# Performance work log

Measured on AMD Instinct MI355X. Metric: run time of the kernel, lower is better.

Reference implementation:

```python
import jax, jax.numpy as jnp
import numpy as np

B, M, KD, VD = 512, 2048, 64, 64
MAX_IT = M - 1  # iteration[0].max().item() in the torch module; made static here


def setup_inputs() -> dict:
    key = jax.random.key(0)
    ks = jax.random.split(key, 8)
    new_key = jax.random.normal(ks[0], (B, KD), dtype=jnp.float32)
    new_value = jax.random.normal(ks[1], (B, VD), dtype=jnp.float32)
    key_memory = jax.random.normal(ks[2], (B, M, KD), dtype=jnp.float32)
    value_memory = jax.random.normal(ks[3], (B, M, VD), dtype=jnp.float32)
    gate = jax.random.normal(ks[4], (B, KD + 1), dtype=jnp.float32)
    iteration = jax.random.randint(ks[5], (B, 1), 1, MAX_IT + 1).astype(jnp.int64 if jax.config.jax_enable_x64 else jnp.int32)
    iteration = iteration.at[0, 0].set(MAX_IT)  # guarantee max == MAX_IT (faithful to .max().item())
    conf_w = jax.random.normal(ks[6], (1, 1), dtype=jnp.float32) * 0.1  # FCNM 1->1 linear weight
    conf_b = jnp.zeros((1,), dtype=jnp.float32)                          # FCNM 1->1 linear bias
    return {
        "new_key": new_key, "new_value": new_value,
        "key_memory": key_memory, "value_memory": value_memory,
        "gate": gate, "conf_w": conf_w, "conf_b": conf_b,
        "iteration": iteration, "max_it": MAX_IT,
    }


def reference(new_key, new_value, key_memory, value_memory, gate, conf_w, conf_b, iteration, max_it):
    b, m, kd = key_memory.shape
    vd = value_memory.shape[-1]
    it = iteration[:, 0]  # [B]

    # --- masked similarity read (vectorized form of the masked_select/scatter_ path) ---
    # memory_mask[b, n] = (n <= iteration[b])
    memory_mask = (jnp.arange(m)[None, :] <= it[:, None]).astype(key_memory.dtype)[..., None]  # [B,M,1]
    not_first = it > 1  # rows where the read actually happens; others stay zero

    vm = value_memory * memory_mask                              # [B,M,VD]
    sim = jnp.einsum('bnd,bd->bn', vm, new_value)                # [B,M]
    wv = jax.nn.softmax(sim, axis=-1)[..., None]                 # [B,M,1]
    conf = jax.nn.sigmoid(sim[..., None] * conf_w[0, 0] + conf_b[0])  # [B,M,1] (1->1 linear + sigmoid)
    km_plus_conf = jnp.concatenate([key_memory, conf], axis=-1)  # [B,M,KD+1]
    read = jnp.sum(wv * km_plus_conf, axis=1)                    # [B,KD+1]
    read = jax.nn.sigmoid(gate) * read
    new_read_key_plus_conf = jnp.where(not_first[:, None], read, jnp.zeros((), dtype=read.dtype))

    # --- resize memory to max_it + 1 slots and scatter-write the new key/value ---
    zeros_k = jnp.zeros((b, 1, kd), dtype=key_memory.dtype)
    zeros_v = jnp.zeros((b, 1, vd), dtype=value_memory.dtype)
    new_key_memory = jnp.concatenate([key_memory[:, :max_it], zeros_k], axis=1)    # [B,max_it+1,KD]
    new_value_memory = jnp.concatenate([value_memory[:, :max_it], zeros_v], axis=1)
    bidx = jnp.arange(b)
    new_key_memory = new_key_memory.at[bidx, it].set(new_key)
    new_value_memory = new_value_memory.at[bidx, it].set(new_value)

    return new_key_memory, new_value_memory, new_read_key_plus_conf
```

## Files before the change

### kernel.cpp

```cpp
#include <hip/hip_runtime.h>
#include <math.h>

#define KD 64
#define VD 64
#define RPB 256
#define RPL 16

typedef float vfloat4 __attribute__((ext_vector_type(4)));

__device__ __forceinline__ vfloat4 ntload4(const float* p) {
    return __builtin_nontemporal_load(reinterpret_cast<const vfloat4*>(p));
}
__device__ __forceinline__ void ntstore4(float* p, vfloat4 v) {
    __builtin_nontemporal_store(v, reinterpret_cast<vfloat4*>(p));
}

__global__ __launch_bounds__(256) void fused_stream(
    const float* __restrict__ value_memory,
    const float* __restrict__ key_memory,
    const float* __restrict__ new_value,
    const float* __restrict__ new_key,
    const int*   __restrict__ iteration,
    const float* __restrict__ conf_w,
    const float* __restrict__ conf_b,
    float* __restrict__ new_value_memory,
    float* __restrict__ new_key_memory,
    float* __restrict__ Spart,
    float* __restrict__ PCpart,
    float* __restrict__ pread,
    int M, int max_it)
{
    const int blocks_per_batch = M / RPB;
    const int b     = blockIdx.x / blocks_per_batch;
    const int split = blockIdx.x % blocks_per_batch;
    const int row0  = split * RPB;
    const int it    = iteration[b];
    const float cw  = conf_w[0], cb = conf_b[0];

    const int tid = threadIdx.x;
    const int l   = tid & 63;
    const int w   = tid >> 6;
    const int c4  = (l & 15) * 4;
    const int rsub = w * 4 + (l >> 4);

    const vfloat4 nv = *reinterpret_cast<const vfloat4*>(new_value + (size_t)b * VD + c4);
    const vfloat4 nk = *reinterpret_cast<const vfloat4*>(new_key   + (size_t)b * KD + c4);
    const float* vmb  = value_memory     + (size_t)b * M * VD;
    const float* kmb  = key_memory       + (size_t)b * M * KD;
    float*       ovmb = new_value_memory + (size_t)b * M * VD;
    float*       okmb = new_key_memory   + (size_t)b * M * KD;

    float sloc = 0.f, pcloc = 0.f;
    vfloat4 acc = (vfloat4){0.f, 0.f, 0.f, 0.f};

    #pragma unroll
    for (int i = 0; i < RPL; ++i) {
        const int n = row0 + rsub + i * 16;
        const size_t off = (size_t)n * 64 + c4;

        vfloat4 v = ntload4(vmb + off);
        vfloat4 k = ntload4(kmb + off);

        float part = fmaf(v.x, nv.x, fmaf(v.y, nv.y, fmaf(v.z, nv.z, v.w * nv.w)));
        part += __shfl_xor(part, 1);
        part += __shfl_xor(part, 2);
        part += __shfl_xor(part, 4);
        part += __shfl_xor(part, 8);

        const float s = (n <= it) ? part : 0.0f;
        const float p = expf(s);
        sloc  += p;
        pcloc += p * (1.0f / (1.0f + expf(-(s * cw + cb))));

        acc.x = fmaf(p, k.x, acc.x); acc.y = fmaf(p, k.y, acc.y);
        acc.z = fmaf(p, k.z, acc.z); acc.w = fmaf(p, k.w, acc.w);

        vfloat4 ovv, ovk;
        if (n == it)          { ovv = nv; ovk = nk; }
        else if (n == max_it) { ovv = (vfloat4){0,0,0,0}; ovk = (vfloat4){0,0,0,0}; }
        else                  { ovv = v;  ovk = k; }
        ntstore4(ovmb + off, ovv);
        ntstore4(okmb + off, ovk);
    }

    sloc  += __shfl_xor(sloc, 16);  sloc  += __shfl_xor(sloc, 32);
    pcloc += __shfl_xor(pcloc, 16); pcloc += __shfl_xor(pcloc, 32);

    acc.x += __shfl_xor(acc.x, 16); acc.y += __shfl_xor(acc.y, 16);
    acc.z += __shfl_xor(acc.z, 16); acc.w += __shfl_xor(acc.w, 16);
    acc.x += __shfl_xor(acc.x, 32); acc.y += __shfl_xor(acc.y, 32);
    acc.z += __shfl_xor(acc.z, 32); acc.w += __shfl_xor(acc.w, 32);

    __shared__ float sS[4], sPC[4];
    __shared__ float racc[4][64];
    if (l == 0) { sS[w] = sloc; sPC[w] = pcloc; }
    if (l < 16) {
        racc[w][c4 + 0] = acc.x; racc[w][c4 + 1] = acc.y;
        racc[w][c4 + 2] = acc.z; racc[w][c4 + 3] = acc.w;
    }
    __syncthreads();
    if (tid == 0) {
        Spart [b * blocks_per_batch + split] = sS[0] + sS[1] + sS[2] + sS[3];
        PCpart[b * blocks_per_batch + split] = sPC[0] + sPC[1] + sPC[2] + sPC[3];
    }
    if (tid < 64) {
        const float sumk = racc[0][tid] + racc[1][tid] + racc[2][tid] + racc[3][tid];
        pread[((size_t)b * blocks_per_batch + split) * 64 + tid] = sumk;
    }
}

__global__ __launch_bounds__(256) void k3_finalize(
    const float* __restrict__ pread,
    const float* __restrict__ Spart,
    const float* __restrict__ PCpart,
    const float* __restrict__ gate,
    const int*   __restrict__ iteration,
    float* __restrict__ out_read,
    int B, int splits)
{
    const int idx = blockIdx.x * 256 + threadIdx.x;
    if (idx >= B * (KD + 1)) return;
    const int b = idx / (KD + 1);
    const int k = idx % (KD + 1);

    float S = 0.f;
    for (int s = 0; s < splits; ++s) S += Spart[b * splits + s];

    float r = 0.f;
    if (k < KD) {
        for (int s = 0; s < splits; ++s)
            r += pread[((size_t)b * splits + s) * 64 + k];
    } else {
        for (int s = 0; s < splits; ++s) r += PCpart[b * splits + s];
    }
    const float g = gate[(size_t)b * (KD + 1) + k];
    float val = (1.0f / (1.0f + expf(-g))) * (r / S);
    if (iteration[b] <= 1) val = 0.0f;
    out_read[idx] = val;
}

extern "C" void kernel_launch(void* const* d_in, const int* in_sizes, int n_in,
                              void* d_out, int out_size, void* d_ws, size_t ws_size,
                              hipStream_t stream) {
    const float* new_key      = (const float*)d_in[0];
    const float* new_value    = (const float*)d_in[1];
    const float* key_memory   = (const float*)d_in[2];
    const float* value_memory = (const float*)d_in[3];
    const float* gate         = (const float*)d_in[4];
    const float* conf_w       = (const float*)d_in[5];
    const float* conf_b       = (const float*)d_in[6];
    const int*   iteration    = (const int*)d_in[7];

    const int B = in_sizes[0] / KD;
    const int M = in_sizes[2] / in_sizes[0];
    const int max_it = M - 1;
    const int splits = M / RPB;

    float* out_km   = (float*)d_out;
    float* out_vm   = out_km + (size_t)B * M * KD;
    float* out_read = out_vm + (size_t)B * M * VD;

    float* Spart  = (float*)d_ws;
    float* PCpart = Spart + (size_t)B * splits;
    float* pread  = PCpart + (size_t)B * splits;

    fused_stream<<<B * splits, 256, 0, stream>>>(
        value_memory, key_memory, new_value, new_key, iteration,
        conf_w, conf_b, out_vm, out_km, Spart, PCpart, pread, M, max_it);

    const int total = B * (KD + 1);
    k3_finalize<<<(total + 255) / 256, 256, 0, stream>>>(
        pread, Spart, PCpart, gate, iteration, out_read, B, splits);
}
```

Before: 204.4 us.

## Fuse read finalize into one block-per-batch streaming kernel with split value/key passes

Replaces the two-kernel split-reduction design with a single kernel that uses one 1024-thread block per batch row, so the softmax normalisation and gate can be applied in-block and the workspace round-trip plus second launch go away. The value memory is streamed first and exp weights are stashed in shared memory, then key memory is streamed in a second loop that reuses them. Scatter writes of new rows and the zero row are peeled out of the loops, and exp/sigmoid switch to fast intrinsics. Only 512 large blocks are launched, with 8KB+ of LDS each, which may limit occupancy and latency hiding relative to the earlier 4096-block grid.

```diff
diff --git a/kernel.cpp b/kernel.cpp
--- a/kernel.cpp
+++ b/kernel.cpp
@@ -3,8 +3,8 @@
 
 #define KD 64
 #define VD 64
-#define RPB 256
-#define RPL 16
+#define MM 2048
+#define NITER (MM / 64)
 
 typedef float vfloat4 __attribute__((ext_vector_type(4)));
 
@@ -14,8 +14,11 @@
 __device__ __forceinline__ void ntstore4(float* p, vfloat4 v) {
     __builtin_nontemporal_store(v, reinterpret_cast<vfloat4*>(p));
 }
+__device__ __forceinline__ float fastsig(float x) {
+    return __builtin_amdgcn_rcpf(1.0f + __expf(-x));
+}
 
-__global__ __launch_bounds__(256) void fused_stream(
+__global__ __launch_bounds__(1024) void fused_all(
     const float* __restrict__ value_memory,
     const float* __restrict__ key_memory,
     const float* __restrict__ new_value,
@@ -23,43 +26,42 @@
     const int*   __restrict__ iteration,
     const float* __restrict__ conf_w,
     const float* __restrict__ conf_b,
+    const float* __restrict__ gate,
     float* __restrict__ new_value_memory,
     float* __restrict__ new_key_memory,
-    float* __restrict__ Spart,
-    float* __restrict__ PCpart,
-    float* __restrict__ pread,
-    int M, int max_it)
+    float* __restrict__ out_read,
+    int max_it)
 {
-    const int blocks_per_batch = M / RPB;
-    const int b     = blockIdx.x / blocks_per_batch;
-    const int split = blockIdx.x % blocks_per_batch;
-    const int row0  = split * RPB;
-    const int it    = iteration[b];
-    const float cw  = conf_w[0], cb = conf_b[0];
-
+    const int b   = blockIdx.x;
     const int tid = threadIdx.x;
     const int l   = tid & 63;
     const int w   = tid >> 6;
     const int c4  = (l & 15) * 4;
-    const int rsub = w * 4 + (l >> 4);
+    const int g   = w * 4 + (l >> 4);
+
+    const int it   = iteration[b];
+    const float cw = conf_w[0], cb = conf_b[0];
+
+    __shared__ float pS[MM];
+    __shared__ float sS[16], sPC[16];
+    __shared__ float racc[16][64];
 
     const vfloat4 nv = *reinterpret_cast<const vfloat4*>(new_value + (size_t)b * VD + c4);
     const vfloat4 nk = *reinterpret_cast<const vfloat4*>(new_key   + (size_t)b * KD + c4);
-    const float* vmb  = value_memory     + (size_t)b * M * VD;
-    const float* kmb  = key_memory       + (size_t)b * M * KD;
-    float*       ovmb = new_value_memory + (size_t)b * M * VD;
-    float*       okmb = new_key_memory   + (size_t)b * M * KD;
+    const vfloat4 z4 = (vfloat4){0.f, 0.f, 0.f, 0.f};
+
+    const size_t base = (size_t)g * 64 + c4;
+    const float* vmb  = value_memory     + (size_t)b * MM * VD;
+    const float* kmb  = key_memory       + (size_t)b * MM * KD;
+    float*       ovmb = new_value_memory + (size_t)b * MM * VD;
+    float*       okmb = new_key_memory   + (size_t)b * MM * KD;
 
     float sloc = 0.f, pcloc = 0.f;
-    vfloat4 acc = (vfloat4){0.f, 0.f, 0.f, 0.f};
-
-    #pragma unroll
-    for (int i = 0; i < RPL; ++i) {
-        const int n = row0 + rsub + i * 16;
-        const size_t off = (size_t)n * 64 + c4;
-
+    #pragma unroll 8
+    for (int i = 0; i < NITER; ++i) {
+        const int n = i * 64 + g;
+        const size_t off = base + (size_t)i * 64 * 64;
         vfloat4 v = ntload4(vmb + off);
-        vfloat4 k = ntload4(kmb + off);
 
         float part = fmaf(v.x, nv.x, fmaf(v.y, nv.y, fmaf(v.z, nv.z, v.w * nv.w)));
         part += __shfl_xor(part, 1);
@@ -68,75 +70,61 @@
         part += __shfl_xor(part, 8);
 
         const float s = (n <= it) ? part : 0.0f;
-        const float p = expf(s);
+        const float p = __expf(s);
+        if ((l & 15) == 0) pS[n] = p;
         sloc  += p;
-        pcloc += p * (1.0f / (1.0f + expf(-(s * cw + cb))));
+        pcloc += p * fastsig(fmaf(s, cw, cb));
 
+        if (n != it && n != max_it) ntstore4(ovmb + off, v);
+    }
+    if (g == 63 && it != max_it) ntstore4(ovmb + (size_t)max_it * 64 + c4, z4);
+    if (g == (it & 63))          ntstore4(ovmb + (size_t)it * 64 + c4, nv);
+
+    vfloat4 acc = z4;
+    #pragma unroll 8
+    for (int i = 0; i < NITER; ++i) {
+        const int n = i * 64 + g;
+        const size_t off = base + (size_t)i * 64 * 64;
+        vfloat4 k = ntload4(kmb + off);
+        const float p = pS[n];
         acc.x = fmaf(p, k.x, acc.x); acc.y = fmaf(p, k.y, acc.y);
         acc.z = fmaf(p, k.z, acc.z); acc.w = fmaf(p, k.w, acc.w);
-
-        vfloat4 ovv, ovk;
-        if (n == it)          { ovv = nv; ovk = nk; }
-        else if (n == max_it) { ovv = (vfloat4){0,0,0,0}; ovk = (vfloat4){0,0,0,0}; }
-        else                  { ovv = v;  ovk = k; }
-        ntstore4(ovmb + off, ovv);
-        ntstore4(okmb + off, ovk);
+        if (n != it && n != max_it) ntstore4(okmb + off, k);
     }
+    if (g == 63 && it != max_it) ntstore4(okmb + (size_t)max_it * 64 + c4, z4);
+    if (g == (it & 63))          ntstore4(okmb + (size_t)it * 64 + c4, nk);
 
     sloc  += __shfl_xor(sloc, 16);  sloc  += __shfl_xor(sloc, 32);
     pcloc += __shfl_xor(pcloc, 16); pcloc += __shfl_xor(pcloc, 32);
-
     acc.x += __shfl_xor(acc.x, 16); acc.y += __shfl_xor(acc.y, 16);
     acc.z += __shfl_xor(acc.z, 16); acc.w += __shfl_xor(acc.w, 16);
     acc.x += __shfl_xor(acc.x, 32); acc.y += __shfl_xor(acc.y, 32);
     acc.z += __shfl_xor(acc.z, 32); acc.w += __shfl_xor(acc.w, 32);
 
-    __shared__ float sS[4], sPC[4];
-    __shared__ float racc[4][64];
     if (l == 0) { sS[w] = sloc; sPC[w] = pcloc; }
     if (l < 16) {
         racc[w][c4 + 0] = acc.x; racc[w][c4 + 1] = acc.y;
         racc[w][c4 + 2] = acc.z; racc[w][c4 + 3] = acc.w;
     }
     __syncthreads();
-    if (tid == 0) {
-        Spart [b * blocks_per_batch + split] = sS[0] + sS[1] + sS[2] + sS[3];
-        PCpart[b * blocks_per_batch + split] = sPC[0] + sPC[1] + sPC[2] + sPC[3];
+
+    if (tid < KD + 1) {
+        float S = 0.f;
+        #pragma unroll
+        for (int ww = 0; ww < 16; ++ww) S += sS[ww];
+        float r = 0.f;
+        if (tid < KD) {
+            #pragma unroll
+            for (int ww = 0; ww < 16; ++ww) r += racc[ww][tid];
+        } else {
+            #pragma unroll
+            for (int ww = 0; ww < 16; ++ww) r += sPC[ww];
+        }
+        const float gt = gate[(size_t)b * (KD + 1) + tid];
+        float val = fastsig(gt) * (r / S);
+        if (it <= 1) val = 0.0f;
+        out_read[(size_t)b * (KD + 1) + tid] = val;
     }
-    if (tid < 64) {
-        const float sumk = racc[0][tid] + racc[1][tid] + racc[2][tid] + racc[3][tid];
-        pread[((size_t)b * blocks_per_batch + split) * 64 + tid] = sumk;
-    }
-}
-
-__global__ __launch_bounds__(256) void k3_finalize(
-    const float* __restrict__ pread,
-    const float* __restrict__ Spart,
-    const float* __restrict__ PCpart,
-    const float* __restrict__ gate,
-    const int*   __restrict__ iteration,
-    float* __restrict__ out_read,
-    int B, int splits)
-{
-    const int idx = blockIdx.x * 256 + threadIdx.x;
-    if (idx >= B * (KD + 1)) return;
-    const int b = idx / (KD + 1);
-    const int k = idx % (KD + 1);
-
-    float S = 0.f;
-    for (int s = 0; s < splits; ++s) S += Spart[b * splits + s];
-
-    float r = 0.f;
-    if (k < KD) {
-        for (int s = 0; s < splits; ++s)
-            r += pread[((size_t)b * splits + s) * 64 + k];
-    } else {
-        for (int s = 0; s < splits; ++s) r += PCpart[b * splits + s];
-    }
-    const float g = gate[(size_t)b * (KD + 1) + k];
-    float val = (1.0f / (1.0f + expf(-g))) * (r / S);
-    if (iteration[b] <= 1) val = 0.0f;
-    out_read[idx] = val;
 }
 
 extern "C" void kernel_launch(void* const* d_in, const int* in_sizes, int n_in,
@@ -154,21 +142,12 @@
     const int B = in_sizes[0] / KD;
     const int M = in_sizes[2] / in_sizes[0];
     const int max_it = M - 1;
-    const int splits = M / RPB;
 
     float* out_km   = (float*)d_out;
     float* out_vm   = out_km + (size_t)B * M * KD;
     float* out_read = out_vm + (size_t)B * M * VD;
 
-    float* Spart  = (float*)d_ws;
-    float* PCpart = Spart + (size_t)B * splits;
-    float* pread  = PCpart + (size_t)B * splits;
-
-    fused_stream<<<B * splits, 256, 0, stream>>>(
+    fused_all<<<B, 1024, 0, stream>>>(
         value_memory, key_memory, new_value, new_key, iteration,
-        conf_w, conf_b, out_vm, out_km, Spart, PCpart, pread, M, max_it);
-
-    const int total = B * (KD + 1);
-    k3_finalize<<<(total + 255) / 256, 256, 0, stream>>>(
-        pread, Spart, PCpart, gate, iteration, out_read, B, splits);
+        conf_w, conf_b, gate, out_vm, out_km, out_read, max_it);
 }
```

Result: faster. 192.9 us (-5.6%).

## Split fused loop into value pass and key pass with LDS-staged weights

Applied to the files above, without the earlier changes.

The single loop that loaded value and key rows together is split into two passes. The first streams the value memory, computes the softmax weights, stores them in shared memory and writes the output value rows. The second streams the key memory, accumulates the weighted keys using the stored weights and writes the output key rows. This lowers register pressure and gives each pass a simpler, longer-unrolled memory stream. Separately, expf and the sigmoid divide are replaced with __expf and a hardware reciprocal, which are less precise.

```diff
diff --git a/kernel.cpp b/kernel.cpp
--- a/kernel.cpp
+++ b/kernel.cpp
@@ -4,7 +4,7 @@
 #define KD 64
 #define VD 64
 #define RPB 256
-#define RPL 16
+#define NIT (RPB / 16)
 
 typedef float vfloat4 __attribute__((ext_vector_type(4)));
 
@@ -13,6 +13,9 @@
 }
 __device__ __forceinline__ void ntstore4(float* p, vfloat4 v) {
     __builtin_nontemporal_store(v, reinterpret_cast<vfloat4*>(p));
+}
+__device__ __forceinline__ float fastsig(float x) {
+    return __builtin_amdgcn_rcpf(1.0f + __expf(-x));
 }
 
 __global__ __launch_bounds__(256) void fused_stream(
@@ -41,25 +44,29 @@
     const int l   = tid & 63;
     const int w   = tid >> 6;
     const int c4  = (l & 15) * 4;
-    const int rsub = w * 4 + (l >> 4);
+    const int g   = w * 4 + (l >> 4);
+
+    __shared__ float pS[RPB];
+    __shared__ float sS[4], sPC[4];
+    __shared__ float racc[4][64];
 
     const vfloat4 nv = *reinterpret_cast<const vfloat4*>(new_value + (size_t)b * VD + c4);
     const vfloat4 nk = *reinterpret_cast<const vfloat4*>(new_key   + (size_t)b * KD + c4);
+    const vfloat4 z4 = (vfloat4){0.f, 0.f, 0.f, 0.f};
+
     const float* vmb  = value_memory     + (size_t)b * M * VD;
     const float* kmb  = key_memory       + (size_t)b * M * KD;
     float*       ovmb = new_value_memory + (size_t)b * M * VD;
     float*       okmb = new_key_memory   + (size_t)b * M * KD;
+    const size_t base = (size_t)(row0 + g) * 64 + c4;
 
     float sloc = 0.f, pcloc = 0.f;
-    vfloat4 acc = (vfloat4){0.f, 0.f, 0.f, 0.f};
-
-    #pragma unroll
-    for (int i = 0; i < RPL; ++i) {
-        const int n = row0 + rsub + i * 16;
-        const size_t off = (size_t)n * 64 + c4;
-
+    #pragma unroll 8
+    for (int i = 0; i < NIT; ++i) {
+        const int r = i * 16 + g;
+        const int n = row0 + r;
+        const size_t off = base + (size_t)i * 16 * 64;
         vfloat4 v = ntload4(vmb + off);
-        vfloat4 k = ntload4(kmb + off);
 
         float part = fmaf(v.x, nv.x, fmaf(v.y, nv.y, fmaf(v.z, nv.z, v.w * nv.w)));
         part += __shfl_xor(part, 1);
@@ -68,31 +75,39 @@
         part += __shfl_xor(part, 8);
 
         const float s = (n <= it) ? part : 0.0f;
-        const float p = expf(s);
+        const float p = __expf(s);
+        if ((l & 15) == 0) pS[r] = p;
         sloc  += p;
-        pcloc += p * (1.0f / (1.0f + expf(-(s * cw + cb))));
+        pcloc += p * fastsig(fmaf(s, cw, cb));
 
+        vfloat4 ov = (n == max_it) ? z4 : v;
+        ov = (n == it) ? nv : ov;
+        ntstore4(ovmb + off, ov);
+    }
+
+    vfloat4 acc = z4;
+    #pragma unroll 16
+    for (int i = 0; i < NIT; ++i) {
+        const int r = i * 16 + g;
+        const int n = row0 + r;
+        const size_t off = base + (size_t)i * 16 * 64;
+        vfloat4 k = ntload4(kmb + off);
+        const float p = pS[r];
         acc.x = fmaf(p, k.x, acc.x); acc.y = fmaf(p, k.y, acc.y);
         acc.z = fmaf(p, k.z, acc.z); acc.w = fmaf(p, k.w, acc.w);
 
-        vfloat4 ovv, ovk;
-        if (n == it)          { ovv = nv; ovk = nk; }
-        else if (n == max_it) { ovv = (vfloat4){0,0,0,0}; ovk = (vfloat4){0,0,0,0}; }
-        else                  { ovv = v;  ovk = k; }
-        ntstore4(ovmb + off, ovv);
-        ntstore4(okmb + off, ovk);
+        vfloat4 ov = (n == max_it) ? z4 : k;
+        ov = (n == it) ? nk : ov;
+        ntstore4(okmb + off, ov);
     }
 
     sloc  += __shfl_xor(sloc, 16);  sloc  += __shfl_xor(sloc, 32);
     pcloc += __shfl_xor(pcloc, 16); pcloc += __shfl_xor(pcloc, 32);
-
     acc.x += __shfl_xor(acc.x, 16); acc.y += __shfl_xor(acc.y, 16);
     acc.z += __shfl_xor(acc.z, 16); acc.w += __shfl_xor(acc.w, 16);
     acc.x += __shfl_xor(acc.x, 32); acc.y += __shfl_xor(acc.y, 32);
     acc.z += __shfl_xor(acc.z, 32); acc.w += __shfl_xor(acc.w, 32);
 
-    __shared__ float sS[4], sPC[4];
-    __shared__ float racc[4][64];
     if (l == 0) { sS[w] = sloc; sPC[w] = pcloc; }
     if (l < 16) {
         racc[w][c4 + 0] = acc.x; racc[w][c4 + 1] = acc.y;
@@ -134,7 +149,7 @@
         for (int s = 0; s < splits; ++s) r += PCpart[b * splits + s];
     }
     const float g = gate[(size_t)b * (KD + 1) + k];
-    float val = (1.0f / (1.0f + expf(-g))) * (r / S);
+    float val = fastsig(g) * (r / S);
     if (iteration[b] <= 1) val = 0.0f;
     out_read[idx] = val;
 }
```

Measured after the change: 202.9 us. No clear change (-0.7%).
